# Optimization experiments

Hardware: AMD Instinct MI355X
Metric: run time of the kernel (lower is better)

Reference implementation:

```python
import jax, jax.numpy as jnp
import numpy as np

B, T, D, H = 256, 2048, 64, 64

def setup_inputs() -> dict:
    key = jax.random.key(0)
    ks = jax.random.split(key, 9)
    s_in = 1.0 / np.sqrt(D)
    s_rec = 1.0 / np.sqrt(H)
    return {
        "lstm_input": jax.random.normal(ks[0], (B, T, D), dtype=jnp.float32),
        "inputs_state": jax.random.normal(ks[1], (B, H), dtype=jnp.float32),
        # LSTM kernel/recurrent_kernel/bias, Keras gate order [i, f, c, o]
        "W": jax.random.normal(ks[2], (D, 4 * H), dtype=jnp.float32) * s_in,
        "U": jax.random.normal(ks[3], (H, 4 * H), dtype=jnp.float32) * s_rec,
        "b": jax.random.normal(ks[4], (4 * H,), dtype=jnp.float32) * 0.05,
        # Dense(1) heads
        "w_gamma": jax.random.normal(ks[5], (H, 1), dtype=jnp.float32) * s_rec,
        "b_gamma": jax.random.normal(ks[6], (1,), dtype=jnp.float32) * 0.05,
        "w_beta": jax.random.normal(ks[7], (H, 1), dtype=jnp.float32) * s_rec,
        "b_beta": jax.random.normal(ks[8], (1,), dtype=jnp.float32) * 0.05,
    }

def reference(lstm_input, inputs_state, W, U, b, w_gamma, b_gamma, w_beta, b_beta):
    # Keras LSTM(64, activation='sigmoid'): recurrent_activation=sigmoid (gates),
    # activation=sigmoid (candidate + cell output, replacing the usual tanh).
    # get_initial_state(inputs_state) -> zero h0/c0 (only batch size is used).
    sig = jax.nn.sigmoid
    # Precompute input projections for all timesteps: [B,T,4H]
    xz = jnp.einsum('btd,dg->btg', lstm_input, W) + b

    def step(carry, z_t):
        h, c = carry
        z = z_t + h @ U  # [B,4H]
        i, f, g, o = jnp.split(z, 4, axis=-1)
        c = sig(f) * c + sig(i) * sig(g)
        h = sig(o) * sig(c)
        return (h, c), None

    h0 = jnp.zeros((lstm_input.shape[0], H), dtype=lstm_input.dtype)
    c0 = jnp.zeros_like(h0)
    (h, _), _ = jax.lax.scan(step, (h0, c0), jnp.swapaxes(xz, 0, 1))

    gamma = h @ w_gamma + b_gamma  # [B,1]
    beta = h @ w_beta + b_beta     # [B,1]
    return (gamma, beta)
```

## Files before the change

### kernel.cpp

```cpp
#include <hip/hip_runtime.h>


typedef _Float16 f16;
typedef f16  half8 __attribute__((ext_vector_type(8)));
typedef float f32x4 __attribute__((ext_vector_type(4)));

constexpr int Bsz = 256;
constexpr int Tn  = 2048;
constexpr int Dn  = 64;
constexpr int G4  = 256;
constexpr int BPB = 4;
constexpr int HSTR = 160;

__global__ __launch_bounds__(256, 1) void lstm_film_mfma(
    const float* __restrict__ x,
    const float* __restrict__ W,
    const float* __restrict__ U,
    const float* __restrict__ bias,
    const float* __restrict__ wg, const float* __restrict__ bgam,
    const float* __restrict__ wb, const float* __restrict__ bbet,
    float* __restrict__ out)
{
    __shared__ __align__(16) char hbuf[2][BPB * HSTR];

    const int tid  = threadIdx.x;
    const int w    = tid >> 6;
    const int l    = tid & 63;
    const int lrow = l & 15;
    const int kgrp = l >> 4;

    const float NK = -1.44269504f;

    half8 Bf[4][4];
#pragma unroll
    for (int kf = 0; kf < 4; ++kf) {
        const float* M = (kf < 2) ? U : W;
        const int krow0 = (kf & 1) * 32 + kgrp * 8;
#pragma unroll
        for (int q = 0; q < 4; ++q) {
            const int col = q * 64 + w * 16 + lrow;
#pragma unroll
            for (int j = 0; j < 8; ++j)
                Bf[kf][q][j] = (f16)(M[(krow0 + j) * G4 + col] * NK);
        }
    }
    float bq[4];
#pragma unroll
    for (int q = 0; q < 4; ++q) bq[q] = bias[q * 64 + w * 16 + lrow] * NK;

    if (tid < (2 * BPB * HSTR) / 16) ((uint4*)hbuf)[tid] = uint4{0, 0, 0, 0};
    float c = 0.0f;

    const float* xlane = x + ((size_t)(blockIdx.x * BPB + (lrow >> 2)) * Tn
                              + (lrow & 3)) * Dn + kgrp * 8;

    const int rdA = (lrow >> 2) * HSTR + kgrp * 16;
    const int rdB = rdA + 64;
    const int wrb = (l >> 4) * HSTR + (w * 16 + lrow) * 2;

    const float wgj = wg[l], wbj = wb[l];
    const float bg0 = bgam[0], bb0 = bbet[0];

    __syncthreads();

#define XL(R, TB) do {                                                       \
        const float* p_ = xlane + (size_t)(TB) * (4 * Dn);                   \
        R[0] = *(const float4*)(p_);      R[1] = *(const float4*)(p_ + 4);   \
        R[2] = *(const float4*)(p_ + 32); R[3] = *(const float4*)(p_ + 36);  \
    } while (0)

    float4 RA[4], RB[4];
    XL(RA, 0); XL(RB, 1);

    f32x4 xzA0, xzA1, xzA2, xzA3, xzB0, xzB1, xzB2, xzB3;

#define XBLOCK(XZ, R, TBN) do {                                              \
        half8 af0, af1;                                                      \
        af0[0]=(f16)R[0].x; af0[1]=(f16)R[0].y; af0[2]=(f16)R[0].z;          \
        af0[3]=(f16)R[0].w; af0[4]=(f16)R[1].x; af0[5]=(f16)R[1].y;          \
        af0[6]=(f16)R[1].z; af0[7]=(f16)R[1].w;                              \
        af1[0]=(f16)R[2].x; af1[1]=(f16)R[2].y; af1[2]=(f16)R[2].z;          \
        af1[3]=(f16)R[2].w; af1[4]=(f16)R[3].x; af1[5]=(f16)R[3].y;          \
        af1[6]=(f16)R[3].z; af1[7]=(f16)R[3].w;                              \
        XL(R, TBN);                             \
        XZ##0 = f32x4{bq[0], bq[0], bq[0], bq[0]};                           \
        XZ##1 = f32x4{bq[1], bq[1], bq[1], bq[1]};                           \
        XZ##2 = f32x4{bq[2], bq[2], bq[2], bq[2]};                           \
        XZ##3 = f32x4{bq[3], bq[3], bq[3], bq[3]};                           \
        XZ##0 = __builtin_amdgcn_mfma_f32_16x16x32_f16(af0, Bf[2][0], XZ##0,0,0,0);\
        XZ##1 = __builtin_amdgcn_mfma_f32_16x16x32_f16(af0, Bf[2][1], XZ##1,0,0,0);\
        XZ##2 = __builtin_amdgcn_mfma_f32_16x16x32_f16(af0, Bf[2][2], XZ##2,0,0,0);\
        XZ##3 = __builtin_amdgcn_mfma_f32_16x16x32_f16(af0, Bf[2][3], XZ##3,0,0,0);\
        XZ##0 = __builtin_amdgcn_mfma_f32_16x16x32_f16(af1, Bf[3][0], XZ##0,0,0,0);\
        XZ##1 = __builtin_amdgcn_mfma_f32_16x16x32_f16(af1, Bf[3][1], XZ##1,0,0,0);\
        XZ##2 = __builtin_amdgcn_mfma_f32_16x16x32_f16(af1, Bf[3][2], XZ##2,0,0,0);\
        XZ##3 = __builtin_amdgcn_mfma_f32_16x16x32_f16(af1, Bf[3][3], XZ##3,0,0,0);\
    } while (0)

#define HSTEP_PRE(P)                                                         \
        asm volatile("s_waitcnt lgkmcnt(0)" ::: "memory");                   \
        __builtin_amdgcn_s_barrier();                                        \
        asm volatile("" ::: "memory");                                       \
        const char* hb_ = hbuf[P];                                           \
        half8 ah0_ = *(const half8*)(hb_ + rdA);                             \
        half8 ah1_ = *(const half8*)(hb_ + rdB);

#define HSTEP_POST(XZ, S, P) do {                                            \
        f32x4 c0 = XZ##0; c0[0] = XZ##0[S];                                  \
        f32x4 c1 = XZ##1; c1[0] = XZ##1[S];                                  \
        f32x4 c2 = XZ##2; c2[0] = XZ##2[S];                                  \
        f32x4 c3 = XZ##3; c3[0] = XZ##3[S];                                  \
        c0 = __builtin_amdgcn_mfma_f32_16x16x32_f16(ah0_, Bf[0][0], c0,0,0,0);\
        c1 = __builtin_amdgcn_mfma_f32_16x16x32_f16(ah0_, Bf[0][1], c1,0,0,0);\
        c2 = __builtin_amdgcn_mfma_f32_16x16x32_f16(ah0_, Bf[0][2], c2,0,0,0);\
        c3 = __builtin_amdgcn_mfma_f32_16x16x32_f16(ah0_, Bf[0][3], c3,0,0,0);\
        c0 = __builtin_amdgcn_mfma_f32_16x16x32_f16(ah1_, Bf[1][0], c0,0,0,0);\
        c1 = __builtin_amdgcn_mfma_f32_16x16x32_f16(ah1_, Bf[1][1], c1,0,0,0);\
        c2 = __builtin_amdgcn_mfma_f32_16x16x32_f16(ah1_, Bf[1][2], c2,0,0,0);\
        c3 = __builtin_amdgcn_mfma_f32_16x16x32_f16(ah1_, Bf[1][3], c3,0,0,0);\
                         \
        const float ei = __builtin_amdgcn_exp2f(c0[0]);                      \
        const float ef = __builtin_amdgcn_exp2f(c1[0]);                      \
        const float eg = __builtin_amdgcn_exp2f(c2[0]);                      \
        const float eo = __builtin_amdgcn_exp2f(c3[0]);                      \
        const float sf  = __builtin_amdgcn_rcpf(1.0f + ef);                  \
        const float sig = __builtin_amdgcn_rcpf((1.0f + ei) * (1.0f + eg));  \
        c = fmaf(sf, c, sig);                                                \
        const float ec = __builtin_amdgcn_exp2f(c * NK);                     \
        const float hh = __builtin_amdgcn_rcpf((1.0f + eo) * (1.0f + ec));   \
        *(f16*)(hbuf[(P) ^ 1] + wrb) = (f16)hh;                              \
    } while (0)

    XBLOCK(xzA, RA, 2);

    constexpr int NTB = Tn / 4;
    for (int tb = 0; tb < NTB; tb += 2) {
        const int tbn0 = tb + 3 < NTB ? tb + 3 : NTB - 1;
        const int tbn1 = tb + 4 < NTB ? tb + 4 : NTB - 1;
        {
            HSTEP_PRE(0)
            XBLOCK(xzB, RB, tbn0);
            HSTEP_POST(xzA, 0, 0);
        }
        { HSTEP_PRE(1) HSTEP_POST(xzA, 1, 1); }
        { HSTEP_PRE(0) HSTEP_POST(xzA, 2, 0); }
        { HSTEP_PRE(1) HSTEP_POST(xzA, 3, 1); }
        {
            HSTEP_PRE(0)
            XBLOCK(xzA, RA, tbn1);
            HSTEP_POST(xzB, 0, 0);
        }
        { HSTEP_PRE(1) HSTEP_POST(xzB, 1, 1); }
        { HSTEP_PRE(0) HSTEP_POST(xzB, 2, 0); }
        { HSTEP_PRE(1) HSTEP_POST(xzB, 3, 1); }
    }
#undef HSTEP_PRE
#undef HSTEP_POST
#undef XBLOCK
#undef XL

    __syncthreads();

    {
        const float hv = (float)*(const f16*)(hbuf[0] + w * HSTR + l * 2);
        float vg = hv * wgj, vb = hv * wbj;
#pragma unroll
        for (int off = 32; off > 0; off >>= 1) {
            vg += __shfl_xor(vg, off, 64);
            vb += __shfl_xor(vb, off, 64);
        }
        if (l == 0) {
            out[blockIdx.x * BPB + w]       = vg + bg0;
            out[Bsz + blockIdx.x * BPB + w] = vb + bb0;
        }
    }
}

extern "C" void kernel_launch(void* const* d_in, const int* in_sizes, int n_in,
                              void* d_out, int out_size, void* d_ws, size_t ws_size,
                              hipStream_t stream) {
    const float* x    = (const float*)d_in[0];
    const float* W    = (const float*)d_in[2];
    const float* U    = (const float*)d_in[3];
    const float* bias = (const float*)d_in[4];
    const float* wg   = (const float*)d_in[5];
    const float* bgam = (const float*)d_in[6];
    const float* wb   = (const float*)d_in[7];
    const float* bbet = (const float*)d_in[8];
    float* out = (float*)d_out;

    lstm_film_mfma<<<Bsz / BPB, 256, 0, stream>>>(x, W, U, bias,
                                                  wg, bgam, wb, bbet, out);
}
```

Before: 461.1 us.

## Map one batch row per block and stage 16-step input projections in LDS

```diff
diff --git a/kernel.cpp b/kernel.cpp
--- a/kernel.cpp
+++ b/kernel.cpp
@@ -3,14 +3,14 @@
 
 typedef _Float16 f16;
 typedef f16  half8 __attribute__((ext_vector_type(8)));
+typedef __fp16 fp16x2 __attribute__((ext_vector_type(2)));
 typedef float f32x4 __attribute__((ext_vector_type(4)));
 
 constexpr int Bsz = 256;
 constexpr int Tn  = 2048;
 constexpr int Dn  = 64;
 constexpr int G4  = 256;
-constexpr int BPB = 4;
-constexpr int HSTR = 160;
+constexpr int XZS = 68;
 
 __global__ __launch_bounds__(256, 1) void lstm_film_mfma(
     const float* __restrict__ x,
@@ -21,7 +21,8 @@
     const float* __restrict__ wb, const float* __restrict__ bbet,
     float* __restrict__ out)
 {
-    __shared__ __align__(16) char hbuf[2][BPB * HSTR];
+    __shared__ __align__(16) char hbuf[2][128];
+    __shared__ __align__(16) float xzbuf[4][2][16][XZS];
 
     const int tid  = threadIdx.x;
     const int w    = tid >> 6;
@@ -48,121 +49,116 @@
 #pragma unroll
     for (int q = 0; q < 4; ++q) bq[q] = bias[q * 64 + w * 16 + lrow] * NK;
 
-    if (tid < (2 * BPB * HSTR) / 16) ((uint4*)hbuf)[tid] = uint4{0, 0, 0, 0};
+    if (tid < 16) ((uint4*)hbuf)[tid] = uint4{0, 0, 0, 0};
     float c = 0.0f;
 
-    const float* xlane = x + ((size_t)(blockIdx.x * BPB + (lrow >> 2)) * Tn
-                              + (lrow & 3)) * Dn + kgrp * 8;
+    const float* xlane = x + ((size_t)blockIdx.x * Tn + lrow) * Dn + kgrp * 8;
 
-    const int rdA = (lrow >> 2) * HSTR + kgrp * 16;
-    const int rdB = rdA + 64;
-    const int wrb = (l >> 4) * HSTR + (w * 16 + lrow) * 2;
+    const int rdH0 = kgrp * 16;
+    const int rdH1 = kgrp * 16 + 64;
+    const int wrH  = (w * 16 + lrow) * 2;
+
+    float* xzw = &xzbuf[w][0][0][0];
 
     const float wgj = wg[l], wbj = wb[l];
     const float bg0 = bgam[0], bb0 = bbet[0];
 
     __syncthreads();
 
-#define XL(R, TB) do {                                                       \
-        const float* p_ = xlane + (size_t)(TB) * (4 * Dn);                   \
+#define XL(R, T0) do {                                                       \
+        const float* p_ = xlane + (size_t)(T0) * Dn;                         \
         R[0] = *(const float4*)(p_);      R[1] = *(const float4*)(p_ + 4);   \
         R[2] = *(const float4*)(p_ + 32); R[3] = *(const float4*)(p_ + 36);  \
     } while (0)
 
-    float4 RA[4], RB[4];
-    XL(RA, 0); XL(RB, 1);
-
-    f32x4 xzA0, xzA1, xzA2, xzA3, xzB0, xzB1, xzB2, xzB3;
-
-#define XBLOCK(XZ, R, TBN) do {                                              \
-        half8 af0, af1;                                                      \
-        af0[0]=(f16)R[0].x; af0[1]=(f16)R[0].y; af0[2]=(f16)R[0].z;          \
-        af0[3]=(f16)R[0].w; af0[4]=(f16)R[1].x; af0[5]=(f16)R[1].y;          \
-        af0[6]=(f16)R[1].z; af0[7]=(f16)R[1].w;                              \
-        af1[0]=(f16)R[2].x; af1[1]=(f16)R[2].y; af1[2]=(f16)R[2].z;          \
-        af1[3]=(f16)R[2].w; af1[4]=(f16)R[3].x; af1[5]=(f16)R[3].y;          \
-        af1[6]=(f16)R[3].z; af1[7]=(f16)R[3].w;                              \
-        XL(R, TBN);                             \
-        XZ##0 = f32x4{bq[0], bq[0], bq[0], bq[0]};                           \
-        XZ##1 = f32x4{bq[1], bq[1], bq[1], bq[1]};                           \
-        XZ##2 = f32x4{bq[2], bq[2], bq[2], bq[2]};                           \
-        XZ##3 = f32x4{bq[3], bq[3], bq[3], bq[3]};                           \
-        XZ##0 = __builtin_amdgcn_mfma_f32_16x16x32_f16(af0, Bf[2][0], XZ##0,0,0,0);\
-        XZ##1 = __builtin_amdgcn_mfma_f32_16x16x32_f16(af0, Bf[2][1], XZ##1,0,0,0);\
-        XZ##2 = __builtin_amdgcn_mfma_f32_16x16x32_f16(af0, Bf[2][2], XZ##2,0,0,0);\
-        XZ##3 = __builtin_amdgcn_mfma_f32_16x16x32_f16(af0, Bf[2][3], XZ##3,0,0,0);\
-        XZ##0 = __builtin_amdgcn_mfma_f32_16x16x32_f16(af1, Bf[3][0], XZ##0,0,0,0);\
-        XZ##1 = __builtin_amdgcn_mfma_f32_16x16x32_f16(af1, Bf[3][1], XZ##1,0,0,0);\
-        XZ##2 = __builtin_amdgcn_mfma_f32_16x16x32_f16(af1, Bf[3][2], XZ##2,0,0,0);\
-        XZ##3 = __builtin_amdgcn_mfma_f32_16x16x32_f16(af1, Bf[3][3], XZ##3,0,0,0);\
+#define XBLOCK(R, X) do {                                                    \
+        union { fp16x2 p[4]; half8 h8; } u0, u1;                             \
+        u0.p[0] = __builtin_amdgcn_cvt_pkrtz(R[0].x, R[0].y);                \
+        u0.p[1] = __builtin_amdgcn_cvt_pkrtz(R[0].z, R[0].w);                \
+        u0.p[2] = __builtin_amdgcn_cvt_pkrtz(R[1].x, R[1].y);                \
+        u0.p[3] = __builtin_amdgcn_cvt_pkrtz(R[1].z, R[1].w);                \
+        u1.p[0] = __builtin_amdgcn_cvt_pkrtz(R[2].x, R[2].y);                \
+        u1.p[1] = __builtin_amdgcn_cvt_pkrtz(R[2].z, R[2].w);                \
+        u1.p[2] = __builtin_amdgcn_cvt_pkrtz(R[3].x, R[3].y);                \
+        u1.p[3] = __builtin_amdgcn_cvt_pkrtz(R[3].z, R[3].w);                \
+        f32x4 q0 = {bq[0], bq[0], bq[0], bq[0]};                             \
+        f32x4 q1 = {bq[1], bq[1], bq[1], bq[1]};                             \
+        f32x4 q2 = {bq[2], bq[2], bq[2], bq[2]};                             \
+        f32x4 q3 = {bq[3], bq[3], bq[3], bq[3]};                             \
+        q0 = __builtin_amdgcn_mfma_f32_16x16x32_f16(u0.h8, Bf[2][0], q0,0,0,0);\
+        q1 = __builtin_amdgcn_mfma_f32_16x16x32_f16(u0.h8, Bf[2][1], q1,0,0,0);\
+        q2 = __builtin_amdgcn_mfma_f32_16x16x32_f16(u0.h8, Bf[2][2], q2,0,0,0);\
+        q3 = __builtin_amdgcn_mfma_f32_16x16x32_f16(u0.h8, Bf[2][3], q3,0,0,0);\
+        q0 = __builtin_amdgcn_mfma_f32_16x16x32_f16(u1.h8, Bf[3][0], q0,0,0,0);\
+        q1 = __builtin_amdgcn_mfma_f32_16x16x32_f16(u1.h8, Bf[3][1], q1,0,0,0);\
+        q2 = __builtin_amdgcn_mfma_f32_16x16x32_f16(u1.h8, Bf[3][2], q2,0,0,0);\
+        q3 = __builtin_amdgcn_mfma_f32_16x16x32_f16(u1.h8, Bf[3][3], q3,0,0,0);\
+        float* bp = xzw + (X) * (16 * XZS);                                  \
+        _Pragma("unroll")                                                    \
+        for (int r = 0; r < 4; ++r) {                                        \
+            f32x4 tv; tv[0] = q0[r]; tv[1] = q1[r];                          \
+            tv[2] = q2[r]; tv[3] = q3[r];                                    \
+            *(f32x4*)(bp + (4 * kgrp + r) * XZS + lrow * 4) = tv;            \
+        }                                                                    \
     } while (0)
 
-#define HSTEP_PRE(P)                                                         \
+#define HSTEP(S, X) do {                                                     \
         asm volatile("s_waitcnt lgkmcnt(0)" ::: "memory");                   \
         __builtin_amdgcn_s_barrier();                                        \
         asm volatile("" ::: "memory");                                       \
-        const char* hb_ = hbuf[P];                                           \
-        half8 ah0_ = *(const half8*)(hb_ + rdA);                             \
-        half8 ah1_ = *(const half8*)(hb_ + rdB);
-
-#define HSTEP_POST(XZ, S, P) do {                                            \
-        f32x4 c0 = XZ##0; c0[0] = XZ##0[S];                                  \
-        f32x4 c1 = XZ##1; c1[0] = XZ##1[S];                                  \
-        f32x4 c2 = XZ##2; c2[0] = XZ##2[S];                                  \
-        f32x4 c3 = XZ##3; c3[0] = XZ##3[S];                                  \
-        c0 = __builtin_amdgcn_mfma_f32_16x16x32_f16(ah0_, Bf[0][0], c0,0,0,0);\
-        c1 = __builtin_amdgcn_mfma_f32_16x16x32_f16(ah0_, Bf[0][1], c1,0,0,0);\
-        c2 = __builtin_amdgcn_mfma_f32_16x16x32_f16(ah0_, Bf[0][2], c2,0,0,0);\
-        c3 = __builtin_amdgcn_mfma_f32_16x16x32_f16(ah0_, Bf[0][3], c3,0,0,0);\
-        c0 = __builtin_amdgcn_mfma_f32_16x16x32_f16(ah1_, Bf[1][0], c0,0,0,0);\
-        c1 = __builtin_amdgcn_mfma_f32_16x16x32_f16(ah1_, Bf[1][1], c1,0,0,0);\
-        c2 = __builtin_amdgcn_mfma_f32_16x16x32_f16(ah1_, Bf[1][2], c2,0,0,0);\
-        c3 = __builtin_amdgcn_mfma_f32_16x16x32_f16(ah1_, Bf[1][3], c3,0,0,0);\
-                         \
-        const float ei = __builtin_amdgcn_exp2f(c0[0]);                      \
-        const float ef = __builtin_amdgcn_exp2f(c1[0]);                      \
-        const float eg = __builtin_amdgcn_exp2f(c2[0]);                      \
-        const float eo = __builtin_amdgcn_exp2f(c3[0]);                      \
+        const char* hb = hbuf[(S) & 1];                                      \
+        half8 ah0 = *(const half8*)(hb + rdH0);                              \
+        half8 ah1 = *(const half8*)(hb + rdH1);                              \
+        f32x4 v = *(const f32x4*)(xzw + (X) * (16 * XZS) + (S) * XZS + lrow * 4);\
+        f32x4 a0 = v;                                                        \
+        f32x4 a1 = v; a1[0] = v[1];                                          \
+        f32x4 a2 = v; a2[0] = v[2];                                          \
+        f32x4 a3 = v; a3[0] = v[3];                                          \
+        a0 = __builtin_amdgcn_mfma_f32_16x16x32_f16(ah0, Bf[0][0], a0,0,0,0);\
+        a1 = __builtin_amdgcn_mfma_f32_16x16x32_f16(ah0, Bf[0][1], a1,0,0,0);\
+        a2 = __builtin_amdgcn_mfma_f32_16x16x32_f16(ah0, Bf[0][2], a2,0,0,0);\
+        a3 = __builtin_amdgcn_mfma_f32_16x16x32_f16(ah0, Bf[0][3], a3,0,0,0);\
+        a0 = __builtin_amdgcn_mfma_f32_16x16x32_f16(ah1, Bf[1][0], a0,0,0,0);\
+        a1 = __builtin_amdgcn_mfma_f32_16x16x32_f16(ah1, Bf[1][1], a1,0,0,0);\
+        a2 = __builtin_amdgcn_mfma_f32_16x16x32_f16(ah1, Bf[1][2], a2,0,0,0);\
+        a3 = __builtin_amdgcn_mfma_f32_16x16x32_f16(ah1, Bf[1][3], a3,0,0,0);\
+        const float ei = __builtin_amdgcn_exp2f(a0[0]);                      \
+        const float ef = __builtin_amdgcn_exp2f(a1[0]);                      \
+        const float eg = __builtin_amdgcn_exp2f(a2[0]);                      \
+        const float eo = __builtin_amdgcn_exp2f(a3[0]);                      \
         const float sf  = __builtin_amdgcn_rcpf(1.0f + ef);                  \
         const float sig = __builtin_amdgcn_rcpf((1.0f + ei) * (1.0f + eg));  \
         c = fmaf(sf, c, sig);                                                \
         const float ec = __builtin_amdgcn_exp2f(c * NK);                     \
         const float hh = __builtin_amdgcn_rcpf((1.0f + eo) * (1.0f + ec));   \
-        *(f16*)(hbuf[(P) ^ 1] + wrb) = (f16)hh;                              \
+        *(f16*)(hbuf[((S) & 1) ^ 1] + wrH) = (f16)hh;                        \
     } while (0)
 
-    XBLOCK(xzA, RA, 2);
+    float4 R[4];
+    XL(R, 0);
+    XBLOCK(R, 0);
+    XL(R, 16);
 
-    constexpr int NTB = Tn / 4;
-    for (int tb = 0; tb < NTB; tb += 2) {
-        const int tbn0 = tb + 3 < NTB ? tb + 3 : NTB - 1;
-        const int tbn1 = tb + 4 < NTB ? tb + 4 : NTB - 1;
-        {
-            HSTEP_PRE(0)
-            XBLOCK(xzB, RB, tbn0);
-            HSTEP_POST(xzA, 0, 0);
+    for (int tb = 0; tb < Tn / 16; ++tb) {
+        const int X = tb & 1;
+#pragma unroll
+        for (int s = 0; s < 16; ++s) {
+            if (s == 14 && tb < Tn / 16 - 1) {
+                XBLOCK(R, X ^ 1);
+                const int tn = (tb + 2) * 16;
+                XL(R, tn < Tn ? tn : Tn - 16);
+            }
+            HSTEP(s, X);
         }
-        { HSTEP_PRE(1) HSTEP_POST(xzA, 1, 1); }
-        { HSTEP_PRE(0) HSTEP_POST(xzA, 2, 0); }
-        { HSTEP_PRE(1) HSTEP_POST(xzA, 3, 1); }
-        {
-            HSTEP_PRE(0)
-            XBLOCK(xzA, RA, tbn1);
-            HSTEP_POST(xzB, 0, 0);
-        }
-        { HSTEP_PRE(1) HSTEP_POST(xzB, 1, 1); }
-        { HSTEP_PRE(0) HSTEP_POST(xzB, 2, 0); }
-        { HSTEP_PRE(1) HSTEP_POST(xzB, 3, 1); }
     }
-#undef HSTEP_PRE
-#undef HSTEP_POST
+#undef HSTEP
 #undef XBLOCK
 #undef XL
 
     __syncthreads();
 
-    {
-        const float hv = (float)*(const f16*)(hbuf[0] + w * HSTR + l * 2);
+    if (w == 0) {
+        const float hv = (float)*(const f16*)(hbuf[0] + l * 2);
         float vg = hv * wgj, vb = hv * wbj;
 #pragma unroll
         for (int off = 32; off > 0; off >>= 1) {
@@ -170,8 +166,8 @@
             vb += __shfl_xor(vb, off, 64);
         }
         if (l == 0) {
-            out[blockIdx.x * BPB + w]       = vg + bg0;
-            out[Bsz + blockIdx.x * BPB + w] = vb + bb0;
+            out[blockIdx.x]       = vg + bg0;
+            out[Bsz + blockIdx.x] = vb + bb0;
         }
     }
 }
@@ -189,6 +185,6 @@
     const float* bbet = (const float*)d_in[8];
     float* out = (float*)d_out;
 
-    lstm_film_mfma<<<Bsz / BPB, 256, 0, stream>>>(x, W, U, bias,
-                                                  wg, bgam, wb, bbet, out);
+    lstm_film_mfma<<<Bsz, 256, 0, stream>>>(x, W, U, bias,
+                                            wg, bgam, wb, bbet, out);
 }
```

After: 502.8 us. +9.0%, slower.
